# Optimization experiments

Measured on AMD Instinct MI355X. Metric: run time of the kernel, lower is better.

Reference implementation:

```python
import jax, jax.numpy as jnp
import numpy as np

DIM = 256
NH = 8
HD = DIM // NH          # 32
KD = HD // 2            # 16, attn_ratio=0.5
SCALE = KD ** -0.5
EPS = 1e-3              # BatchNorm2d eps=0.001
B, H, W = 8, 32, 32


def _bn(x, g, b, m, v):
    # inference-mode BatchNorm2d over channel axis 1 of NCHW
    inv = g / jnp.sqrt(v + EPS)
    return x * inv[None, :, None, None] + (b - m * inv)[None, :, None, None]


def setup_inputs() -> dict:
    key = jax.random.key(0)
    ks = jax.random.split(key, 16)
    h_out = DIM + 2 * NH * KD  # 512
    return {
        "x": jax.random.normal(ks[0], (B, DIM, H, W), jnp.float32),
        "qkv_w": jax.random.normal(ks[1], (h_out, DIM), jnp.float32) * 0.05,
        "qkv_g": jax.random.uniform(ks[2], (h_out,), jnp.float32, 0.5, 1.5),
        "qkv_b": jax.random.normal(ks[3], (h_out,), jnp.float32) * 0.1,
        "qkv_m": jax.random.normal(ks[4], (h_out,), jnp.float32) * 0.1,
        "qkv_v": jax.random.uniform(ks[5], (h_out,), jnp.float32, 0.5, 1.5),
        "pe_w": jax.random.normal(ks[6], (DIM, 1, 3, 3), jnp.float32) * 0.1,
        "pe_g": jax.random.uniform(ks[7], (DIM,), jnp.float32, 0.5, 1.5),
        "pe_b": jax.random.normal(ks[8], (DIM,), jnp.float32) * 0.1,
        "pe_m": jax.random.normal(ks[9], (DIM,), jnp.float32) * 0.1,
        "pe_v": jax.random.uniform(ks[10], (DIM,), jnp.float32, 0.5, 1.5),
        "proj_w": jax.random.normal(ks[11], (DIM, DIM), jnp.float32) * 0.05,
        "proj_g": jax.random.uniform(ks[12], (DIM,), jnp.float32, 0.5, 1.5),
        "proj_b": jax.random.normal(ks[13], (DIM,), jnp.float32) * 0.1,
        "proj_m": jax.random.normal(ks[14], (DIM,), jnp.float32) * 0.1,
        "proj_v": jax.random.uniform(ks[15], (DIM,), jnp.float32, 0.5, 1.5),
    }


def reference(x, qkv_w, qkv_g, qkv_b, qkv_m, qkv_v,
              pe_w, pe_g, pe_b, pe_m, pe_v,
              proj_w, proj_g, proj_b, proj_m, proj_v):
    b, c, h, w = x.shape
    n = h * w
    # qkv: 1x1 conv (no bias) + BN, act=Identity
    qkv = _bn(jnp.einsum('oc,bchw->bohw', qkv_w, x), qkv_g, qkv_b, qkv_m, qkv_v)
    qkv = qkv.reshape(b, NH, 2 * KD + HD, n)
    q, k, v = jnp.split(qkv, [KD, 2 * KD], axis=2)  # [b,nh,kd,n],[b,nh,kd,n],[b,nh,hd,n]
    # attn = q^T @ k * scale, softmax over keys (last dim)
    attn = jax.nn.softmax(jnp.einsum('bhkn,bhkm->bhnm', q, k) * SCALE, axis=-1)
    # v @ attn^T -> [b,nh,hd,n]
    out = jnp.einsum('bhdj,bhij->bhdi', v, attn).reshape(b, c, h, w)
    # depthwise 3x3 positional branch on v (reshaped to spatial)
    v_sp = v.reshape(b, c, h, w)
    pe = jax.lax.conv_general_dilated(v_sp, pe_w, window_strides=(1, 1),
                                      padding=((1, 1), (1, 1)),
                                      feature_group_count=c)
    pe = _bn(pe, pe_g, pe_b, pe_m, pe_v)
    x_attn = out + pe
    # final 1x1 projection + BN
    return _bn(jnp.einsum('oc,bchw->bohw', proj_w, x_attn),
               proj_g, proj_b, proj_m, proj_v)
```

## Files before the change

kernel.cpp:

```cpp
#include <hip/hip_runtime.h>
#include <hip/hip_bf16.h>

#define B_    8
#define DIM_  256
#define NH_   8
#define HD_   32
#define KD_   16
#define HOUT_ 512
#define N_    1024
#define SCALE_ 0.25f
#define EPS_  1e-3f

typedef unsigned short u16;
typedef __attribute__((ext_vector_type(8))) short short8;
typedef __attribute__((ext_vector_type(4))) float f32x4;

union Frag { short8 v; u16 e[8]; };
union H4   { uint2 u; u16 e[4]; };

__device__ __forceinline__ float b2f(u16 u) {
    union { unsigned int i; float f; } c;
    c.i = ((unsigned int)u) << 16;
    return c.f;
}

__device__ __forceinline__ u16 f2b(float f) {
    union { float f; unsigned int i; } c;
    c.f = f;
    unsigned int x = c.i;
    return (u16)((x + 0x7fffu + ((x >> 16) & 1u)) >> 16);
}

__global__ __launch_bounds__(256) void k_prep(
    const float* __restrict__ qw, const float* __restrict__ pw,
    const float* __restrict__ qg, const float* __restrict__ qb,
    const float* __restrict__ qm, const float* __restrict__ qv,
    const float* __restrict__ pg, const float* __restrict__ pb,
    const float* __restrict__ pm, const float* __restrict__ pv,
    u16* __restrict__ wq_bf, u16* __restrict__ wp_bf,
    float2* __restrict__ bnq, float2* __restrict__ bnp)
{
    int i = blockIdx.x * 256 + threadIdx.x;
    wq_bf[i] = f2b(qw[i]);
    if (i < 65536) wp_bf[i] = f2b(pw[i]);
    if (i < 512) {
        float inv = qg[i] / sqrtf(qv[i] + EPS_);
        bnq[i] = make_float2(inv, qb[i] - qm[i] * inv);
    } else if (i < 768) {
        int o = i - 512;
        float inv = pg[o] / sqrtf(pv[o] + EPS_);
        bnp[o] = make_float2(inv, pb[o] - pm[o] * inv);
    }
}

__global__ __launch_bounds__(256) void k_qkv(
    const float* __restrict__ x, const u16* __restrict__ wbf,
    const float2* __restrict__ bn, u16* __restrict__ qkv)
{
    int blk = blockIdx.x;
    int nb = blk & 7, ob = (blk >> 3) & 7, b = blk >> 6;
    int t = threadIdx.x;
    int wv_ = t >> 6, lane = t & 63, quad = lane >> 4, l16 = lane & 15;
    int o_base = ob * 64 + (wv_ & 1) * 32;
    int n_base = nb * 128 + (wv_ >> 1) * 64;

    f32x4 acc[2][4];
    #pragma unroll
    for (int ot = 0; ot < 2; ++ot)
        #pragma unroll
        for (int nt = 0; nt < 4; ++nt) acc[ot][nt] = (f32x4){0.f, 0.f, 0.f, 0.f};

    const float* xb = x + (size_t)b * DIM_ * N_;
    for (int c0 = 0; c0 < DIM_; c0 += 32) {
        short8 af[2];
        #pragma unroll
        for (int ot = 0; ot < 2; ++ot)
            af[ot] = *(const short8*)(wbf + (size_t)(o_base + ot * 16 + l16) * DIM_ + c0 + quad * 8);
        Frag bf[4];
        #pragma unroll
        for (int nt = 0; nt < 4; ++nt) {
            const float* xc = xb + (size_t)(c0 + quad * 8) * N_ + n_base + nt * 16 + l16;
            #pragma unroll
            for (int j = 0; j < 8; ++j) bf[nt].e[j] = f2b(xc[(size_t)j * N_]);
        }
        #pragma unroll
        for (int ot = 0; ot < 2; ++ot)
            #pragma unroll
            for (int nt = 0; nt < 4; ++nt)
                acc[ot][nt] = __builtin_amdgcn_mfma_f32_16x16x32_bf16(af[ot], bf[nt].v, acc[ot][nt], 0, 0, 0);
    }
    #pragma unroll
    for (int ot = 0; ot < 2; ++ot)
        #pragma unroll
        for (int r = 0; r < 4; ++r) {
            int o = o_base + ot * 16 + quad * 4 + r;
            float2 ib = bn[o];
            u16* dst = qkv + (size_t)(b * HOUT_ + o) * N_ + n_base + l16;
            #pragma unroll
            for (int nt = 0; nt < 4; ++nt)
                dst[nt * 16] = f2b(acc[ot][nt][r] * ib.x + ib.y);
        }
}

__global__ __launch_bounds__(256) void k_attn(
    const u16* __restrict__ qkv, float* __restrict__ xattn)
{
    __shared__ u16   q_t[64][24];
    __shared__ u16   k_t[256][24];
    __shared__ u16   p_s[4][16][80];
    __shared__ float o_s[4][32][17];

    int blk = blockIdx.x;
    int qb = blk & 15;
    int h  = (blk >> 4) & 7;
    int b  = blk >> 7;
    int t    = threadIdx.x;
    int wv_  = t >> 6;
    int lane = t & 63;
    int quad = lane >> 4;
    int l16  = lane & 15;
    const u16* base = qkv + (size_t)(b * HOUT_ + h * 64) * N_;

    {
        int q = t & 63, d4 = (t >> 6) * 4;
        H4 hh;
        #pragma unroll
        for (int i = 0; i < 4; ++i)
            hh.e[i] = f2b(b2f(base[(size_t)(d4 + i) * N_ + qb * 64 + q]) * SCALE_);
        *(uint2*)&q_t[q][d4] = hh.u;
    }
    __syncthreads();

    short8 qf = {0, 0, 0, 0, 0, 0, 0, 0};
    if (quad < 2) qf = *(const short8*)&q_t[wv_ * 16 + l16][quad * 8];

    f32x4 oa0 = {0.f, 0.f, 0.f, 0.f};
    f32x4 oa1 = {0.f, 0.f, 0.f, 0.f};
    float l_acc[4] = {0.f, 0.f, 0.f, 0.f};

    for (int ch = 0; ch < 4; ++ch) {
        int ch0 = ch * 256;
        __syncthreads();
        {
            #pragma unroll
            for (int d4 = 0; d4 < 16; d4 += 4) {
                H4 hh;
                #pragma unroll
                for (int i = 0; i < 4; ++i)
                    hh.e[i] = base[(size_t)(16 + d4 + i) * N_ + ch0 + t];
                *(uint2*)&k_t[t][d4] = hh.u;
            }
        }
        __syncthreads();

        for (int kt = 0; kt < 4; ++kt) {
            int key0 = ch0 + kt * 64;
            #pragma unroll
            for (int nt = 0; nt < 4; ++nt) {
                short8 kf = {0, 0, 0, 0, 0, 0, 0, 0};
                if (quad < 2) kf = *(const short8*)&k_t[kt * 64 + nt * 16 + l16][quad * 8];
                f32x4 zero = {0.f, 0.f, 0.f, 0.f};
                f32x4 s = __builtin_amdgcn_mfma_f32_16x16x32_bf16(qf, kf, zero, 0, 0, 0);
                #pragma unroll
                for (int r = 0; r < 4; ++r) {
                    float p = __expf(fminf(s[r], 80.f));
                    l_acc[r] += p;
                    p_s[wv_][quad * 4 + r][nt * 16 + l16] = f2b(p);
                }
            }
            #pragma unroll
            for (int kc = 0; kc < 2; ++kc) {
                short8 pf = *(const short8*)&p_s[wv_][l16][kc * 32 + quad * 8];
                {
                    const u16* vsrc = base + (size_t)(32 + l16) * N_ + key0 + kc * 32 + quad * 8;
                    short8 vf = *(const short8*)vsrc;
                    oa0 = __builtin_amdgcn_mfma_f32_16x16x32_bf16(pf, vf, oa0, 0, 0, 0);
                }
                {
                    const u16* vsrc = base + (size_t)(48 + l16) * N_ + key0 + kc * 32 + quad * 8;
                    short8 vf = *(const short8*)vsrc;
                    oa1 = __builtin_amdgcn_mfma_f32_16x16x32_bf16(pf, vf, oa1, 0, 0, 0);
                }
            }
        }
    }

    #pragma unroll
    for (int r = 0; r < 4; ++r) {
        float v = l_acc[r];
        v += __shfl_xor(v, 1);
        v += __shfl_xor(v, 2);
        v += __shfl_xor(v, 4);
        v += __shfl_xor(v, 8);
        l_acc[r] = v;
    }
    #pragma unroll
    for (int r = 0; r < 4; ++r) {
        o_s[wv_][l16][quad * 4 + r]      = oa0[r] / l_acc[r];
        o_s[wv_][16 + l16][quad * 4 + r] = oa1[r] / l_acc[r];
    }
    {
        int d = lane >> 1, qo = (lane & 1) * 8;
        float* dst = xattn + (size_t)(b * DIM_ + h * HD_ + d) * N_ + qb * 64 + wv_ * 16 + qo;
        float4 r0, r1;
        r0.x = o_s[wv_][d][qo + 0]; r0.y = o_s[wv_][d][qo + 1];
        r0.z = o_s[wv_][d][qo + 2]; r0.w = o_s[wv_][d][qo + 3];
        r1.x = o_s[wv_][d][qo + 4]; r1.y = o_s[wv_][d][qo + 5];
        r1.z = o_s[wv_][d][qo + 6]; r1.w = o_s[wv_][d][qo + 7];
        ((float4*)dst)[0] = r0;
        ((float4*)dst)[1] = r1;
    }
}

__global__ __launch_bounds__(256) void k_pe(
    const u16* __restrict__ qkv, const float* __restrict__ pw,
    const float* __restrict__ g, const float* __restrict__ bb,
    const float* __restrict__ mm, const float* __restrict__ vv,
    float* __restrict__ xattn)
{
    int idx = blockIdx.x * 256 + threadIdx.x;
    int n = idx & 1023;
    int c = (idx >> 10) & 255;
    int b = idx >> 18;
    int h = c >> 5, d = c & 31;

    const u16* vrow = qkv + (size_t)(b * HOUT_ + h * 64 + 32 + d) * N_;
    int y = n >> 5, x0 = n & 31;
    float s = 0.f;
    #pragma unroll
    for (int dy = -1; dy <= 1; ++dy) {
        int yy = y + dy;
        if (yy < 0 || yy > 31) continue;
        #pragma unroll
        for (int dx = -1; dx <= 1; ++dx) {
            int xx = x0 + dx;
            if (xx < 0 || xx > 31) continue;
            s += pw[c * 9 + (dy + 1) * 3 + (dx + 1)] * b2f(vrow[yy * 32 + xx]);
        }
    }
    float inv = g[c] / sqrtf(vv[c] + EPS_);
    xattn[idx] += s * inv + (bb[c] - mm[c] * inv);
}

__global__ __launch_bounds__(256) void k_proj(
    const float* __restrict__ xattn, const u16* __restrict__ wbf,
    const float2* __restrict__ bn, float* __restrict__ out)
{
    int blk = blockIdx.x;
    int nb = blk & 7, ob = (blk >> 3) & 3, b = blk >> 5;
    int t = threadIdx.x;
    int wv_ = t >> 6, lane = t & 63, quad = lane >> 4, l16 = lane & 15;
    int o_base = ob * 64 + (wv_ & 1) * 32;
    int n_base = nb * 128 + (wv_ >> 1) * 64;

    f32x4 acc[2][4];
    #pragma unroll
    for (int ot = 0; ot < 2; ++ot)
        #pragma unroll
        for (int nt = 0; nt < 4; ++nt) acc[ot][nt] = (f32x4){0.f, 0.f, 0.f, 0.f};

    const float* xb = xattn + (size_t)b * DIM_ * N_;
    for (int c0 = 0; c0 < DIM_; c0 += 32) {
        short8 af[2];
        #pragma unroll
        for (int ot = 0; ot < 2; ++ot)
            af[ot] = *(const short8*)(wbf + (size_t)(o_base + ot * 16 + l16) * DIM_ + c0 + quad * 8);
        Frag bf[4];
        #pragma unroll
        for (int nt = 0; nt < 4; ++nt) {
            const float* xc = xb + (size_t)(c0 + quad * 8) * N_ + n_base + nt * 16 + l16;
            #pragma unroll
            for (int j = 0; j < 8; ++j) bf[nt].e[j] = f2b(xc[(size_t)j * N_]);
        }
        #pragma unroll
        for (int ot = 0; ot < 2; ++ot)
            #pragma unroll
            for (int nt = 0; nt < 4; ++nt)
                acc[ot][nt] = __builtin_amdgcn_mfma_f32_16x16x32_bf16(af[ot], bf[nt].v, acc[ot][nt], 0, 0, 0);
    }
    #pragma unroll
    for (int ot = 0; ot < 2; ++ot)
        #pragma unroll
        for (int r = 0; r < 4; ++r) {
            int o = o_base + ot * 16 + quad * 4 + r;
            float2 ib = bn[o];
            float* dst = out + (size_t)(b * DIM_ + o) * N_ + n_base + l16;
            #pragma unroll
            for (int nt = 0; nt < 4; ++nt)
                dst[nt * 16] = acc[ot][nt][r] * ib.x + ib.y;
        }
}

extern "C" void kernel_launch(void* const* d_in, const int* in_sizes, int n_in,
                              void* d_out, int out_size, void* d_ws, size_t ws_size,
                              hipStream_t stream)
{
    const float* x      = (const float*)d_in[0];
    const float* qkv_w  = (const float*)d_in[1];
    const float* qkv_g  = (const float*)d_in[2];
    const float* qkv_b  = (const float*)d_in[3];
    const float* qkv_m  = (const float*)d_in[4];
    const float* qkv_v  = (const float*)d_in[5];
    const float* pe_w   = (const float*)d_in[6];
    const float* pe_g   = (const float*)d_in[7];
    const float* pe_b   = (const float*)d_in[8];
    const float* pe_m   = (const float*)d_in[9];
    const float* pe_v   = (const float*)d_in[10];
    const float* proj_w = (const float*)d_in[11];
    const float* proj_g = (const float*)d_in[12];
    const float* proj_b = (const float*)d_in[13];
    const float* proj_m = (const float*)d_in[14];
    const float* proj_v = (const float*)d_in[15];
    float* out = (float*)d_out;

    char* p = (char*)d_ws;
    u16*    qkv   = (u16*)p;          p += (size_t)B_ * HOUT_ * N_ * sizeof(u16);
    float*  xattn = (float*)p;        p += (size_t)B_ * DIM_ * N_ * sizeof(float);
    u16*    wq_bf = (u16*)p;          p += (size_t)HOUT_ * DIM_ * sizeof(u16);
    u16*    wp_bf = (u16*)p;          p += (size_t)DIM_ * DIM_ * sizeof(u16);
    float2* bnq   = (float2*)p;       p += 512 * sizeof(float2);
    float2* bnp   = (float2*)p;

    hipLaunchKernelGGL(k_prep, dim3(512), dim3(256), 0, stream,
                       qkv_w, proj_w, qkv_g, qkv_b, qkv_m, qkv_v,
                       proj_g, proj_b, proj_m, proj_v, wq_bf, wp_bf, bnq, bnp);
    hipLaunchKernelGGL(k_qkv, dim3(512), dim3(256), 0, stream,
                       x, wq_bf, bnq, qkv);
    hipLaunchKernelGGL(k_attn, dim3(B_ * NH_ * 16), dim3(256), 0, stream,
                       qkv, xattn);
    hipLaunchKernelGGL(k_pe, dim3(B_ * DIM_ * N_ / 256), dim3(256), 0, stream,
                       qkv, pe_w, pe_g, pe_b, pe_m, pe_v, xattn);
    hipLaunchKernelGGL(k_proj, dim3(256), dim3(256), 0, stream,
                       xattn, wp_bf, bnp, out);
}
```

Before: 169.9 us.

## Fuse depthwise PE conv into attention and use transposed bf16 GEMM inputs

Folds the depthwise 3x3 positional-encoding conv and its BatchNorm into the attention kernel's epilogue, staging the needed V rows in shared memory and removing the separate k_pe pass with its read-modify-write of xattn. Attention output is now written as bf16 in [b,n,c] layout so the projection GEMM can load contiguous short8 fragments. A new transpose kernel does the same for x before the QKV GEMM, replacing strided fp32 gathers with vector loads. The trade is an extra launch and round trip for xT, an extra barrier and shared-memory union in k_attn, and a bf16-rounded intermediate that k_proj already rounded to before.

```diff
diff --git a/kernel.cpp b/kernel.cpp
--- a/kernel.cpp
+++ b/kernel.cpp
@@ -15,8 +15,7 @@
 typedef __attribute__((ext_vector_type(8))) short short8;
 typedef __attribute__((ext_vector_type(4))) float f32x4;
 
-union Frag { short8 v; u16 e[8]; };
-union H4   { uint2 u; u16 e[4]; };
+union H4 { uint2 u; u16 e[4]; };
 
 __device__ __forceinline__ float b2f(u16 u) {
     union { unsigned int i; float f; } c;
@@ -33,12 +32,16 @@
 
 __global__ __launch_bounds__(256) void k_prep(
     const float* __restrict__ qw, const float* __restrict__ pw,
+    const float* __restrict__ pew,
     const float* __restrict__ qg, const float* __restrict__ qb,
     const float* __restrict__ qm, const float* __restrict__ qv,
     const float* __restrict__ pg, const float* __restrict__ pb,
     const float* __restrict__ pm, const float* __restrict__ pv,
+    const float* __restrict__ eg, const float* __restrict__ eb,
+    const float* __restrict__ em, const float* __restrict__ ev,
     u16* __restrict__ wq_bf, u16* __restrict__ wp_bf,
-    float2* __restrict__ bnq, float2* __restrict__ bnp)
+    float2* __restrict__ bnq, float2* __restrict__ bnp,
+    float* __restrict__ wpe, float* __restrict__ bnpe)
 {
     int i = blockIdx.x * 256 + threadIdx.x;
     wq_bf[i] = f2b(qw[i]);
@@ -51,10 +54,39 @@
         float inv = pg[o] / sqrtf(pv[o] + EPS_);
         bnp[o] = make_float2(inv, pb[o] - pm[o] * inv);
     }
+    if (i < 2304) {
+        int c = i / 9;
+        float inv = eg[c] / sqrtf(ev[c] + EPS_);
+        wpe[i] = pew[i] * inv;
+        if (i % 9 == 0) bnpe[c] = eb[c] - em[c] * inv;
+    }
+}
+
+__global__ __launch_bounds__(256) void k_xt(
+    const float* __restrict__ x, u16* __restrict__ xT)
+{
+    __shared__ float t_s[64][65];
+    int blk = blockIdx.x;
+    int nt = blk & 15, ct = (blk >> 4) & 3, b = blk >> 6;
+    int t = threadIdx.x;
+    int c0 = ct * 64, n0 = nt * 64;
+    #pragma unroll
+    for (int i = 0; i < 16; ++i) {
+        int idx = i * 256 + t;
+        int c = idx >> 6, n = idx & 63;
+        t_s[n][c] = x[(size_t)(b * DIM_ + c0 + c) * N_ + n0 + n];
+    }
+    __syncthreads();
+    #pragma unroll
+    for (int i = 0; i < 16; ++i) {
+        int idx = i * 256 + t;
+        int n = idx >> 6, c = idx & 63;
+        xT[(size_t)(b * N_ + n0 + n) * DIM_ + c0 + c] = f2b(t_s[n][c]);
+    }
 }
 
 __global__ __launch_bounds__(256) void k_qkv(
-    const float* __restrict__ x, const u16* __restrict__ wbf,
+    const u16* __restrict__ xT, const u16* __restrict__ wbf,
     const float2* __restrict__ bn, u16* __restrict__ qkv)
 {
     int blk = blockIdx.x;
@@ -70,24 +102,21 @@
         #pragma unroll
         for (int nt = 0; nt < 4; ++nt) acc[ot][nt] = (f32x4){0.f, 0.f, 0.f, 0.f};
 
-    const float* xb = x + (size_t)b * DIM_ * N_;
+    const u16* xb = xT + (size_t)b * N_ * DIM_;
     for (int c0 = 0; c0 < DIM_; c0 += 32) {
         short8 af[2];
         #pragma unroll
         for (int ot = 0; ot < 2; ++ot)
             af[ot] = *(const short8*)(wbf + (size_t)(o_base + ot * 16 + l16) * DIM_ + c0 + quad * 8);
-        Frag bf[4];
-        #pragma unroll
-        for (int nt = 0; nt < 4; ++nt) {
-            const float* xc = xb + (size_t)(c0 + quad * 8) * N_ + n_base + nt * 16 + l16;
-            #pragma unroll
-            for (int j = 0; j < 8; ++j) bf[nt].e[j] = f2b(xc[(size_t)j * N_]);
-        }
+        short8 bf[4];
+        #pragma unroll
+        for (int nt = 0; nt < 4; ++nt)
+            bf[nt] = *(const short8*)(xb + (size_t)(n_base + nt * 16 + l16) * DIM_ + c0 + quad * 8);
         #pragma unroll
         for (int ot = 0; ot < 2; ++ot)
             #pragma unroll
             for (int nt = 0; nt < 4; ++nt)
-                acc[ot][nt] = __builtin_amdgcn_mfma_f32_16x16x32_bf16(af[ot], bf[nt].v, acc[ot][nt], 0, 0, 0);
+                acc[ot][nt] = __builtin_amdgcn_mfma_f32_16x16x32_bf16(af[ot], bf[nt], acc[ot][nt], 0, 0, 0);
     }
     #pragma unroll
     for (int ot = 0; ot < 2; ++ot)
@@ -102,12 +131,15 @@
         }
 }
 
+struct MainSmem { u16 k_t[256][24]; u16 p_s[4][16][80]; };
+union  SmemU    { MainSmem m; float v_pe[128][33]; };
+
 __global__ __launch_bounds__(256) void k_attn(
-    const u16* __restrict__ qkv, float* __restrict__ xattn)
-{
+    const u16* __restrict__ qkv, const float* __restrict__ wpe,
+    const float* __restrict__ bnpe, u16* __restrict__ xattnT)
+{
+    __shared__ SmemU su;
     __shared__ u16   q_t[64][24];
-    __shared__ u16   k_t[256][24];
-    __shared__ u16   p_s[4][16][80];
     __shared__ float o_s[4][32][17];
 
     int blk = blockIdx.x;
@@ -148,7 +180,7 @@
                 #pragma unroll
                 for (int i = 0; i < 4; ++i)
                     hh.e[i] = base[(size_t)(16 + d4 + i) * N_ + ch0 + t];
-                *(uint2*)&k_t[t][d4] = hh.u;
+                *(uint2*)&su.m.k_t[t][d4] = hh.u;
             }
         }
         __syncthreads();
@@ -158,28 +190,26 @@
             #pragma unroll
             for (int nt = 0; nt < 4; ++nt) {
                 short8 kf = {0, 0, 0, 0, 0, 0, 0, 0};
-                if (quad < 2) kf = *(const short8*)&k_t[kt * 64 + nt * 16 + l16][quad * 8];
+                if (quad < 2) kf = *(const short8*)&su.m.k_t[kt * 64 + nt * 16 + l16][quad * 8];
                 f32x4 zero = {0.f, 0.f, 0.f, 0.f};
                 f32x4 s = __builtin_amdgcn_mfma_f32_16x16x32_bf16(qf, kf, zero, 0, 0, 0);
                 #pragma unroll
                 for (int r = 0; r < 4; ++r) {
                     float p = __expf(fminf(s[r], 80.f));
                     l_acc[r] += p;
-                    p_s[wv_][quad * 4 + r][nt * 16 + l16] = f2b(p);
+                    su.m.p_s[wv_][quad * 4 + r][nt * 16 + l16] = f2b(p);
                 }
             }
             #pragma unroll
             for (int kc = 0; kc < 2; ++kc) {
-                short8 pf = *(const short8*)&p_s[wv_][l16][kc * 32 + quad * 8];
+                short8 pf = *(const short8*)&su.m.p_s[wv_][l16][kc * 32 + quad * 8];
                 {
                     const u16* vsrc = base + (size_t)(32 + l16) * N_ + key0 + kc * 32 + quad * 8;
-                    short8 vf = *(const short8*)vsrc;
-                    oa0 = __builtin_amdgcn_mfma_f32_16x16x32_bf16(pf, vf, oa0, 0, 0, 0);
+                    oa0 = __builtin_amdgcn_mfma_f32_16x16x32_bf16(pf, *(const short8*)vsrc, oa0, 0, 0, 0);
                 }
                 {
                     const u16* vsrc = base + (size_t)(48 + l16) * N_ + key0 + kc * 32 + quad * 8;
-                    short8 vf = *(const short8*)vsrc;
-                    oa1 = __builtin_amdgcn_mfma_f32_16x16x32_bf16(pf, vf, oa1, 0, 0, 0);
+                    oa1 = __builtin_amdgcn_mfma_f32_16x16x32_bf16(pf, *(const short8*)vsrc, oa1, 0, 0, 0);
                 }
             }
         }
@@ -199,51 +229,52 @@
         o_s[wv_][l16][quad * 4 + r]      = oa0[r] / l_acc[r];
         o_s[wv_][16 + l16][quad * 4 + r] = oa1[r] / l_acc[r];
     }
+    __syncthreads();
+
     {
-        int d = lane >> 1, qo = (lane & 1) * 8;
-        float* dst = xattn + (size_t)(b * DIM_ + h * HD_ + d) * N_ + qb * 64 + wv_ * 16 + qo;
-        float4 r0, r1;
-        r0.x = o_s[wv_][d][qo + 0]; r0.y = o_s[wv_][d][qo + 1];
-        r0.z = o_s[wv_][d][qo + 2]; r0.w = o_s[wv_][d][qo + 3];
-        r1.x = o_s[wv_][d][qo + 4]; r1.y = o_s[wv_][d][qo + 5];
-        r1.z = o_s[wv_][d][qo + 6]; r1.w = o_s[wv_][d][qo + 7];
-        ((float4*)dst)[0] = r0;
-        ((float4*)dst)[1] = r1;
-    }
-}
-
-__global__ __launch_bounds__(256) void k_pe(
-    const u16* __restrict__ qkv, const float* __restrict__ pw,
-    const float* __restrict__ g, const float* __restrict__ bb,
-    const float* __restrict__ mm, const float* __restrict__ vv,
-    float* __restrict__ xattn)
-{
-    int idx = blockIdx.x * 256 + threadIdx.x;
-    int n = idx & 1023;
-    int c = (idx >> 10) & 255;
-    int b = idx >> 18;
-    int h = c >> 5, d = c & 31;
-
-    const u16* vrow = qkv + (size_t)(b * HOUT_ + h * 64 + 32 + d) * N_;
-    int y = n >> 5, x0 = n & 31;
-    float s = 0.f;
-    #pragma unroll
-    for (int dy = -1; dy <= 1; ++dy) {
-        int yy = y + dy;
-        if (yy < 0 || yy > 31) continue;
-        #pragma unroll
-        for (int dx = -1; dx <= 1; ++dx) {
-            int xx = x0 + dx;
-            if (xx < 0 || xx > 31) continue;
-            s += pw[c * 9 + (dy + 1) * 3 + (dx + 1)] * b2f(vrow[yy * 32 + xx]);
-        }
-    }
-    float inv = g[c] / sqrtf(vv[c] + EPS_);
-    xattn[idx] += s * inv + (bb[c] - mm[c] * inv);
+        int ybase = qb * 2 - 1;
+        #pragma unroll
+        for (int i = 0; i < 16; ++i) {
+            int idx = i * 256 + t;
+            int d = idx >> 7, px = idx & 127;
+            int y = ybase + (px >> 5);
+            float v = 0.f;
+            if (y >= 0 && y < 32)
+                v = b2f(base[(size_t)(32 + d) * N_ + y * 32 + (px & 31)]);
+            su.v_pe[px][d] = v;
+        }
+    }
+    __syncthreads();
+
+    {
+        int d = t & 31, pxg = t >> 5;
+        int c = h * 32 + d;
+        float w9[9];
+        #pragma unroll
+        for (int k = 0; k < 9; ++k) w9[k] = wpe[c * 9 + k];
+        float beta = bnpe[c];
+        #pragma unroll
+        for (int ii = 0; ii < 8; ++ii) {
+            int pl = pxg * 8 + ii;
+            int xx0 = pl & 31;
+            float s = beta;
+            #pragma unroll
+            for (int dy = -1; dy <= 1; ++dy) {
+                #pragma unroll
+                for (int dx = -1; dx <= 1; ++dx) {
+                    int xx = xx0 + dx;
+                    if (xx < 0 || xx > 31) continue;
+                    s += w9[(dy + 1) * 3 + (dx + 1)] * su.v_pe[pl + 32 + dy * 32 + dx][d];
+                }
+            }
+            float o = o_s[pl >> 4][d][pl & 15];
+            xattnT[(size_t)(b * N_ + qb * 64 + pl) * DIM_ + c] = f2b(o + s);
+        }
+    }
 }
 
 __global__ __launch_bounds__(256) void k_proj(
-    const float* __restrict__ xattn, const u16* __restrict__ wbf,
+    const u16* __restrict__ xattnT, const u16* __restrict__ wbf,
     const float2* __restrict__ bn, float* __restrict__ out)
 {
     int blk = blockIdx.x;
@@ -259,24 +290,21 @@
         #pragma unroll
         for (int nt = 0; nt < 4; ++nt) acc[ot][nt] = (f32x4){0.f, 0.f, 0.f, 0.f};
 
-    const float* xb = xattn + (size_t)b * DIM_ * N_;
+    const u16* xb = xattnT + (size_t)b * N_ * DIM_;
     for (int c0 = 0; c0 < DIM_; c0 += 32) {
         short8 af[2];
         #pragma unroll
         for (int ot = 0; ot < 2; ++ot)
             af[ot] = *(const short8*)(wbf + (size_t)(o_base + ot * 16 + l16) * DIM_ + c0 + quad * 8);
-        Frag bf[4];
-        #pragma unroll
-        for (int nt = 0; nt < 4; ++nt) {
-            const float* xc = xb + (size_t)(c0 + quad * 8) * N_ + n_base + nt * 16 + l16;
-            #pragma unroll
-            for (int j = 0; j < 8; ++j) bf[nt].e[j] = f2b(xc[(size_t)j * N_]);
-        }
+        short8 bf[4];
+        #pragma unroll
+        for (int nt = 0; nt < 4; ++nt)
+            bf[nt] = *(const short8*)(xb + (size_t)(n_base + nt * 16 + l16) * DIM_ + c0 + quad * 8);
         #pragma unroll
         for (int ot = 0; ot < 2; ++ot)
             #pragma unroll
             for (int nt = 0; nt < 4; ++nt)
-                acc[ot][nt] = __builtin_amdgcn_mfma_f32_16x16x32_bf16(af[ot], bf[nt].v, acc[ot][nt], 0, 0, 0);
+                acc[ot][nt] = __builtin_amdgcn_mfma_f32_16x16x32_bf16(af[ot], bf[nt], acc[ot][nt], 0, 0, 0);
     }
     #pragma unroll
     for (int ot = 0; ot < 2; ++ot)
@@ -314,22 +342,27 @@
     float* out = (float*)d_out;
 
     char* p = (char*)d_ws;
-    u16*    qkv   = (u16*)p;          p += (size_t)B_ * HOUT_ * N_ * sizeof(u16);
-    float*  xattn = (float*)p;        p += (size_t)B_ * DIM_ * N_ * sizeof(float);
-    u16*    wq_bf = (u16*)p;          p += (size_t)HOUT_ * DIM_ * sizeof(u16);
-    u16*    wp_bf = (u16*)p;          p += (size_t)DIM_ * DIM_ * sizeof(u16);
-    float2* bnq   = (float2*)p;       p += 512 * sizeof(float2);
-    float2* bnp   = (float2*)p;
+    u16*    qkv    = (u16*)p;    p += (size_t)B_ * HOUT_ * N_ * sizeof(u16);
+    u16*    xT     = (u16*)p;    p += (size_t)B_ * N_ * DIM_ * sizeof(u16);
+    u16*    xattnT = (u16*)p;    p += (size_t)B_ * N_ * DIM_ * sizeof(u16);
+    u16*    wq_bf  = (u16*)p;    p += (size_t)HOUT_ * DIM_ * sizeof(u16);
+    u16*    wp_bf  = (u16*)p;    p += (size_t)DIM_ * DIM_ * sizeof(u16);
+    float2* bnq    = (float2*)p; p += 512 * sizeof(float2);
+    float2* bnp    = (float2*)p; p += 256 * sizeof(float2);
+    float*  wpe    = (float*)p;  p += 2304 * sizeof(float);
+    float*  bnpe   = (float*)p;
 
     hipLaunchKernelGGL(k_prep, dim3(512), dim3(256), 0, stream,
-                       qkv_w, proj_w, qkv_g, qkv_b, qkv_m, qkv_v,
-                       proj_g, proj_b, proj_m, proj_v, wq_bf, wp_bf, bnq, bnp);
+                       qkv_w, proj_w, pe_w,
+                       qkv_g, qkv_b, qkv_m, qkv_v,
+                       proj_g, proj_b, proj_m, proj_v,
+                       pe_g, pe_b, pe_m, pe_v,
+                       wq_bf, wp_bf, bnq, bnp, wpe, bnpe);
+    hipLaunchKernelGGL(k_xt, dim3(512), dim3(256), 0, stream, x, xT);
     hipLaunchKernelGGL(k_qkv, dim3(512), dim3(256), 0, stream,
-                       x, wq_bf, bnq, qkv);
+                       xT, wq_bf, bnq, qkv);
     hipLaunchKernelGGL(k_attn, dim3(B_ * NH_ * 16), dim3(256), 0, stream,
-                       qkv, xattn);
-    hipLaunchKernelGGL(k_pe, dim3(B_ * DIM_ * N_ / 256), dim3(256), 0, stream,
-                       qkv, pe_w, pe_g, pe_b, pe_m, pe_v, xattn);
+                       qkv, wpe, bnpe, xattnT);
     hipLaunchKernelGGL(k_proj, dim3(256), dim3(256), 0, stream,
-                       xattn, wp_bf, bnp, out);
-}
+                       xattnT, wp_bf, bnp, out);
+}
```

Result: faster. 159.5 us (-6.1%).
